# Performance work log

Hardware: AMD Instinct MI355X
Metric: run time of the kernel (lower is better)

Reference implementation:

```python
import jax, jax.numpy as jnp
import numpy as np

N = 100000      # nodes
E = 3200000     # edges (before self-loops)
F_IN = 512      # input features
HID = 16        # hidden dim (hard-coded in module)
C = 40          # classes
EPS = 1e-12     # F.normalize clamp


def setup_inputs() -> dict:
    key = jax.random.key(0)
    ks = jax.random.split(key, 5)
    x = jax.random.normal(ks[0], (N, F_IN), dtype=jnp.float32)
    edge_index = jax.random.randint(ks[1], (2, E), 0, N, dtype=jnp.int32)
    W1 = jax.random.normal(ks[2], (F_IN, HID), dtype=jnp.float32) / np.sqrt(F_IN)
    b1 = jnp.zeros((HID,), jnp.float32)
    W2 = jax.random.normal(ks[3], (HID, C), dtype=jnp.float32) / np.sqrt(HID)
    b2 = jnp.zeros((C,), jnp.float32)
    beta2 = jnp.ones((), jnp.float32)  # learnable beta of prop2 (init 1.0)
    return {"x": x, "edge_index": edge_index, "W1": W1, "b1": b1,
            "W2": W2, "b2": b2, "beta2": beta2}


def agnn_prop(x, src, dst, beta):
    # x: [N, d]; src/dst: [E'] with self-loops already appended
    norm = jnp.sqrt(jnp.sum(x * x, axis=-1, keepdims=True))
    xn = x / jnp.maximum(norm, EPS)                      # L2 normalize
    alpha = beta * jnp.sum(xn[src] * xn[dst], axis=-1)   # [E'] cosine sim * beta
    # segment softmax over edges grouped by destination node
    amax = jax.ops.segment_max(alpha, dst, num_segments=N)
    amax = jax.lax.stop_gradient(amax)
    ex = jnp.exp(alpha - amax[dst])
    denom = jax.ops.segment_sum(ex, dst, num_segments=N)
    w = ex / denom[dst]                                  # [E']
    return jax.ops.segment_sum(w[:, None] * x[src], dst, num_segments=N)


def reference(x, edge_index, W1, b1, W2, b2, beta2):
    # dropout is identity in eval mode
    h = jax.nn.relu(x @ W1 + b1)                         # [N, 16]
    loops = jnp.arange(N, dtype=edge_index.dtype)
    src = jnp.concatenate([edge_index[0], loops])        # add self-loops (PyG default)
    dst = jnp.concatenate([edge_index[1], loops])
    h = agnn_prop(h, src, dst, jnp.float32(1.0))         # prop1: fixed beta=1
    h = agnn_prop(h, src, dst, beta2)                    # prop2: learnable beta
    logits = h @ W2 + b2                                 # [N, 40]
    return jax.nn.log_softmax(logits, axis=-1)
```

## Files before the change

### kernel.cpp

```cpp
#include <hip/hip_runtime.h>
#include <hip/hip_bf16.h>

#define FIN 512
#define HID 16
#define NCLS 40
#define MAXNB 1024
#define NBLK 256

typedef unsigned short u16;
typedef __attribute__((ext_vector_type(8))) short short8;
typedef __attribute__((ext_vector_type(4))) float f32x4;

__device__ __forceinline__ float bf2f(u16 u) {
    return __uint_as_float(((unsigned int)u) << 16);
}
__device__ __forceinline__ u16 f2bf_rne(float f) {
    unsigned int u = __float_as_uint(f);
    unsigned int r = u + 0x7FFFu + ((u >> 16) & 1u);
    return (u16)(r >> 16);
}
__device__ __forceinline__ float load_in(const void* p, size_t i, int isf32) {
    return isf32 ? ((const float*)p)[i] : bf2f(((const u16*)p)[i]);
}

__global__ void probe_kernel(const unsigned int* __restrict__ x, int* __restrict__ flag)
{
    int cnt = 0;
    for (int i = threadIdx.x; i < 256; i += 64) {
        unsigned int w = x[i];
        float v = __uint_as_float((w & 0xFFFFu) << 16);
        float a = fabsf(v);
        if (a >= 6.1e-5f && a <= 64.f) cnt++;
    }
    #pragma unroll
    for (int off = 32; off >= 1; off >>= 1) cnt += __shfl_xor(cnt, off, 64);
    if (threadIdx.x == 0) *flag = (cnt < 128) ? 1 : 0;
}

__global__ __launch_bounds__(256) void gemm1_mfma(
    const void* __restrict__ x, const void* __restrict__ W1, const void* __restrict__ b1,
    float* __restrict__ h, float* __restrict__ rn, int ngroups, int N,
    const int* __restrict__ flagp)
{
    const int isf32 = *flagp;
    __shared__ u16 w1s[8192];
    __shared__ float b1s[HID];
    const int lane = threadIdx.x & 63;
    const int m    = lane & 15;
    const int quad = lane >> 4;

    for (int i = threadIdx.x; i < 8192; i += 256) {
        int kb = i >> 9, rem = i & 511, ln = rem >> 3, j = rem & 7;
        int k = kb*32 + (ln >> 4)*8 + j;
        w1s[i] = f2bf_rne(load_in(W1, (size_t)k*HID + (ln & 15), isf32));
    }
    if (threadIdx.x < HID) b1s[threadIdx.x] = load_in(b1, threadIdx.x, isf32);
    __syncthreads();

    const int wid = blockIdx.x * 4 + (threadIdx.x >> 6);
    const int nw  = gridDim.x * 4;
    const float bias = b1s[m];

    for (int g = wid; g < ngroups; g += nw) {
        size_t row = (size_t)g*16 + m;
        if (row >= (size_t)N) row = N - 1;
        f32x4 acc = {0.f, 0.f, 0.f, 0.f};
        if (isf32) {
            const float* xb = (const float*)x + row*FIN + quad*8;
            #pragma unroll
            for (int kb = 0; kb < 16; ++kb) {
                f32x4 v0 = *(const f32x4*)(xb + kb*32);
                f32x4 v1 = *(const f32x4*)(xb + kb*32 + 4);
                short8 a;
                a[0] = (short)f2bf_rne(v0[0]); a[1] = (short)f2bf_rne(v0[1]);
                a[2] = (short)f2bf_rne(v0[2]); a[3] = (short)f2bf_rne(v0[3]);
                a[4] = (short)f2bf_rne(v1[0]); a[5] = (short)f2bf_rne(v1[1]);
                a[6] = (short)f2bf_rne(v1[2]); a[7] = (short)f2bf_rne(v1[3]);
                short8 bf = *(const short8*)&w1s[kb*512 + lane*8];
                acc = __builtin_amdgcn_mfma_f32_16x16x32_bf16(a, bf, acc, 0, 0, 0);
            }
        } else {
            const u16* xb = (const u16*)x + row*FIN + quad*8;
            #pragma unroll
            for (int kb = 0; kb < 16; ++kb) {
                short8 a = *(const short8*)(xb + kb*32);
                short8 bf = *(const short8*)&w1s[kb*512 + lane*8];
                acc = __builtin_amdgcn_mfma_f32_16x16x32_bf16(a, bf, acc, 0, 0, 0);
            }
        }
        #pragma unroll
        for (int i = 0; i < 4; ++i) {
            int r = quad*4 + i;
            float v = fmaxf(acc[i] + bias, 0.f);
            size_t orow = (size_t)g*16 + r;
            if (orow < (size_t)N) h[orow*HID + m] = v;
            float ss = v*v;
            ss += __shfl_xor(ss, 1, 64);
            ss += __shfl_xor(ss, 2, 64);
            ss += __shfl_xor(ss, 4, 64);
            ss += __shfl_xor(ss, 8, 64);
            if (m == 0 && orow < (size_t)N) rn[orow] = 1.0f / fmaxf(sqrtf(ss), 1e-12f);
        }
    }
}

__global__ __launch_bounds__(256) void hist2d_kernel(
    const int* __restrict__ dst, int* __restrict__ blkhist, int E, int NB)
{
    __shared__ int hist[MAXNB];
    int t = threadIdx.x;
    for (int i = t; i < NB; i += 256) hist[i] = 0;
    __syncthreads();
    int chunk = (E + gridDim.x - 1) / gridDim.x;
    int beg = blockIdx.x * chunk;
    int end = min(E, beg + chunk);
    for (int i = beg + t; i < end; i += 256)
        atomicAdd(&hist[dst[i] >> 7], 1);
    __syncthreads();
    for (int i = t; i < NB; i += 256)
        blkhist[blockIdx.x * NB + i] = hist[i];
}

__global__ __launch_bounds__(256) void scanB_kernel(
    int* __restrict__ blkhist, int* __restrict__ bcnt, int NB)
{
    int b = blockIdx.x * 4 + (threadIdx.x >> 6);
    if (b >= NB) return;
    int lane = threadIdx.x & 63;
    int run = 0;
    for (int i0 = 0; i0 < NBLK; i0 += 64) {
        int idx = (i0 + lane) * NB + b;
        int v = blkhist[idx];
        int s = v;
        #pragma unroll
        for (int d = 1; d <= 32; d <<= 1) {
            int u = __shfl_up(s, d, 64);
            if (lane >= d) s += u;
        }
        blkhist[idx] = run + s - v;
        run += __shfl(s, 63, 64);
    }
    if (lane == 0) bcnt[b] = run;
}

__global__ __launch_bounds__(1024) void scan_kernel(
    const int* __restrict__ in, int* __restrict__ out, int n)
{
    __shared__ int buf[1024];
    __shared__ int carry;
    int t = threadIdx.x;
    if (t == 0) carry = 0;
    __syncthreads();
    for (int base = 0; base < n; base += 1024) {
        int v = (base + t < n) ? in[base + t] : 0;
        buf[t] = v;
        __syncthreads();
        for (int d = 1; d < 1024; d <<= 1) {
            int x = (t >= d) ? buf[t - d] : 0;
            __syncthreads();
            buf[t] += x;
            __syncthreads();
        }
        if (base + t < n) out[base + t] = carry + buf[t] - v;
        __syncthreads();
        if (t == 0) carry += buf[1023];
        __syncthreads();
    }
}

__global__ __launch_bounds__(256) void scatter_part_kernel(
    const int* __restrict__ src, const int* __restrict__ dst,
    const int* __restrict__ bbase, const int* __restrict__ blkhist,
    int* __restrict__ pairs, int E, int NB)
{
    __shared__ int base[MAXNB];
    __shared__ int cur[MAXNB];
    int t = threadIdx.x;
    for (int i = t; i < NB; i += 256) {
        base[i] = bbase[i] + blkhist[blockIdx.x * NB + i];
        cur[i] = 0;
    }
    __syncthreads();
    int chunk = (E + gridDim.x - 1) / gridDim.x;
    int beg = blockIdx.x * chunk;
    int end = min(E, beg + chunk);
    for (int i = beg + t; i < end; i += 256) {
        int d = dst[i], s = src[i];
        int b = d >> 7;
        int r = atomicAdd(&cur[b], 1);
        pairs[base[b] + r] = ((d & 127) << 24) | s;
    }
}

__global__ __launch_bounds__(256) void bucket_fill_kernel(
    const int* __restrict__ pairs, const int* __restrict__ bbase,
    const int* __restrict__ bcnt, int* __restrict__ row_start,
    int* __restrict__ counts, int* __restrict__ csr, int N)
{
    int b = blockIdx.x, n0 = b << 7;
    __shared__ int lhist[128], loff[128], lcur[128];
    int t = threadIdx.x;
    if (t < 128) { lhist[t] = 0; lcur[t] = 0; }
    __syncthreads();
    int base = bbase[b], cnt = bcnt[b];
    for (int i = t; i < cnt; i += 256)
        atomicAdd(&lhist[((unsigned)pairs[base + i]) >> 24], 1);
    __syncthreads();
    if (t < 64) {
        int c0 = lhist[2*t], c1 = lhist[2*t + 1];
        int tp = c0 + c1, s = tp;
        #pragma unroll
        for (int d = 1; d <= 32; d <<= 1) {
            int u = __shfl_up(s, d, 64);
            if (t >= d) s += u;
        }
        int excl = s - tp;
        loff[2*t] = excl; loff[2*t + 1] = excl + c0;
        int na = n0 + 2*t, nb2 = na + 1;
        if (na < N)  { row_start[na]  = base + excl;      counts[na]  = c0; }
        if (nb2 < N) { row_start[nb2] = base + excl + c0; counts[nb2] = c1; }
    }
    __syncthreads();
    for (int i = t; i < cnt; i += 256) {
        int w = pairs[base + i];
        int s = w & 0xFFFFFF, l = ((unsigned)w) >> 24;
        int p = atomicAdd(&lcur[l], 1);
        csr[base + loff[l] + p] = s;
    }
}

__global__ __launch_bounds__(256) void count_kernel(
    const int* __restrict__ dst, int* __restrict__ counts, int E)
{
    int e = blockIdx.x * 256 + threadIdx.x;
    if (e < E) atomicAdd(&counts[dst[e]], 1);
}

__global__ __launch_bounds__(256) void alloc_kernel(
    const int* __restrict__ counts, int* __restrict__ row_start,
    int* __restrict__ gcur, int N)
{
    int n = blockIdx.x * 256 + threadIdx.x;
    int lane = threadIdx.x & 63;
    int cnt = (n < N) ? counts[n] : 0;
    int s = cnt;
    #pragma unroll
    for (int d = 1; d <= 32; d <<= 1) {
        int t = __shfl_up(s, d, 64);
        if (lane >= d) s += t;
    }
    int total = __shfl(s, 63, 64);
    int base = 0;
    if (lane == 0) base = atomicAdd(gcur, total);
    base = __shfl(base, 0, 64);
    if (n < N) row_start[n] = base + s - cnt;
}

__global__ __launch_bounds__(256) void fill_kernel(
    const int* __restrict__ src, const int* __restrict__ dst,
    const int* __restrict__ row_start, int* __restrict__ cursor,
    int* __restrict__ csr, int E)
{
    int e = blockIdx.x * 256 + threadIdx.x;
    if (e < E) {
        int d = dst[e];
        int p = atomicAdd(&cursor[d], 1);
        csr[row_start[d] + p] = src[e];
    }
}

__global__ __launch_bounds__(256) void prop_kernel(
    const float* __restrict__ f, const float* __restrict__ rn,
    const int* __restrict__ row_start, const int* __restrict__ counts,
    const int* __restrict__ csr, const void* __restrict__ beta_ptr, int use_beta,
    float* __restrict__ out, float* __restrict__ rn_out, int N,
    const int* __restrict__ flagp)
{
    int wid = blockIdx.x * 4 + (threadIdx.x >> 6);
    if (wid >= N) return;
    const int isf32 = *flagp;
    const int lane = threadIdx.x & 63;
    const int sub  = lane & 3;
    const int es   = lane >> 2;
    const int n = wid;

    const float beta = use_beta ? load_in(beta_ptr, 0, isf32) : 1.0f;
    const float M = fabsf(beta);
    const f32x4 fn_v = *(const f32x4*)&f[(size_t)n*HID + sub*4];
    const float rn_n = rn[n];
    const int base = row_start[n];
    const int deg  = counts[n];

    f32x4 acc = {0.f, 0.f, 0.f, 0.f};
    float s = 0.f;
    for (int j0 = 0; j0 < deg + 1; j0 += 16) {
        int j = j0 + es;
        int idx = base + ((j < deg) ? j : 0);
        int v = csr[idx];
        int src = (j < deg) ? v : n;
        f32x4 fs = *(const f32x4*)&f[(size_t)src*HID + sub*4];
        float rs = rn[src];
        float p = fs[0]*fn_v[0] + fs[1]*fn_v[1] + fs[2]*fn_v[2] + fs[3]*fn_v[3];
        p += __shfl_xor(p, 1, 64);
        p += __shfl_xor(p, 2, 64);
        float alpha = beta * p * rs * rn_n;
        float t = (j <= deg) ? __expf(alpha - M) : 0.f;
        s += t;
        acc[0] += t*fs[0]; acc[1] += t*fs[1];
        acc[2] += t*fs[2]; acc[3] += t*fs[3];
    }
    #pragma unroll
    for (int off = 4; off <= 32; off <<= 1) {
        s      += __shfl_xor(s,      off, 64);
        acc[0] += __shfl_xor(acc[0], off, 64);
        acc[1] += __shfl_xor(acc[1], off, 64);
        acc[2] += __shfl_xor(acc[2], off, 64);
        acc[3] += __shfl_xor(acc[3], off, 64);
    }
    f32x4 o;
    o[0] = acc[0]/s; o[1] = acc[1]/s; o[2] = acc[2]/s; o[3] = acc[3]/s;
    if (lane < 4) *(f32x4*)&out[(size_t)n*HID + sub*4] = o;
    float p2 = o[0]*o[0] + o[1]*o[1] + o[2]*o[2] + o[3]*o[3];
    p2 += __shfl_xor(p2, 1, 64);
    p2 += __shfl_xor(p2, 2, 64);
    if (lane == 0) rn_out[n] = 1.0f / fmaxf(sqrtf(p2), 1e-12f);
}

__global__ __launch_bounds__(256) void classify_kernel(
    const float* __restrict__ h2, const void* __restrict__ W2,
    const void* __restrict__ b2, void* __restrict__ out, int N,
    const int* __restrict__ flagp)
{
    const int isf32 = *flagp;
    __shared__ float w2s[HID * NCLS];
    __shared__ float b2s[NCLS];
    for (int i = threadIdx.x; i < HID * NCLS; i += 256) w2s[i] = load_in(W2, i, isf32);
    if (threadIdx.x < NCLS) b2s[threadIdx.x] = load_in(b2, threadIdx.x, isf32);
    __syncthreads();

    int wid = blockIdx.x * 4 + (threadIdx.x >> 6);
    if (wid >= N) return;
    const int lane = threadIdx.x & 63;
    const int n = wid;

    float acc = -3.0e38f;
    if (lane < NCLS) {
        acc = b2s[lane];
        #pragma unroll
        for (int k = 0; k < HID; ++k)
            acc += h2[(size_t)n*HID + k] * w2s[k*NCLS + lane];
    }
    float mx = acc;
    #pragma unroll
    for (int off = 32; off >= 1; off >>= 1)
        mx = fmaxf(mx, __shfl_xor(mx, off, 64));
    float e = (lane < NCLS) ? __expf(acc - mx) : 0.f;
    float sum = e;
    #pragma unroll
    for (int off = 32; off >= 1; off >>= 1)
        sum += __shfl_xor(sum, off, 64);
    if (lane < NCLS) {
        float res = acc - mx - __logf(sum);
        if (!(res == res) || fabsf(res) > 1e30f) res = 0.f;
        size_t oi = (size_t)n*NCLS + lane;
        if (isf32) ((float*)out)[oi] = res;
        else       ((u16*)out)[oi]  = f2bf_rne(res);
    }
}

extern "C" void kernel_launch(void* const* d_in, const int* in_sizes, int n_in,
                              void* d_out, int out_size, void* d_ws, size_t ws_size,
                              hipStream_t stream)
{
    const void* x     = d_in[0];
    const int*  ei    = (const int*)d_in[1];
    const void* W1    = d_in[2];
    const void* b1    = d_in[3];
    const void* W2    = d_in[4];
    const void* b2    = d_in[5];
    const void* beta2 = d_in[6];

    const int N = in_sizes[0] / FIN;
    const int E = in_sizes[1] / 2;
    const int NB = (N + 127) >> 7;
    const int* srcv = ei;
    const int* dstv = ei + E;

    char* ws = (char*)d_ws;
    size_t off = 0;
    auto take = [&](size_t bytes) -> char* {
        char* p = ws + off;
        off += (bytes + 255) & ~(size_t)255;
        return p;
    };
    float* h0        = (float*)take((size_t)N * HID * 4);
    float* rn0       = (float*)take((size_t)N * 4);
    int*   counts    = (int*)take((size_t)N * 4);
    int*   cursor    = (int*)take((size_t)N * 4);
    int*   gcur      = (int*)take(256);
    int*   row_start = (int*)take((size_t)N * 4);
    int*   bcnt      = (int*)take((size_t)NB * 4);
    int*   bbase     = (int*)take((size_t)NB * 4);
    int*   csr       = (int*)take((size_t)(E + 64) * 4);
    int*   flag      = (int*)take(256);
    int*   pairs     = (int*)take((size_t)(E + 64) * 4);
    int*   blkhist   = (int*)take((size_t)NBLK * NB * 4);
    const int use_bucket = (off <= ws_size && NB <= MAXNB && N <= (1 << 24)) ? 1 : 0;

    float* h1  = (float*)d_out;
    float* rn1 = (float*)((char*)d_out + (size_t)N * HID * 4);
    float* h2  = h0;
    float* rn2 = rn0;

    size_t zbytes = (size_t)((char*)gcur - (char*)counts) + 256;
    hipMemsetAsync(counts, 0, zbytes, stream);

    probe_kernel<<<1, 64, 0, stream>>>((const unsigned int*)x, flag);

    const int ngroups = (N + 15) / 16;
    gemm1_mfma<<<(ngroups + 3) / 4, 256, 0, stream>>>(x, W1, b1, h0, rn0, ngroups, N, flag);

    int eb = (E + 255) / 256;
    int nb = (N + 255) / 256;
    int wb = (N + 3) / 4;
    if (use_bucket) {
        hist2d_kernel<<<NBLK, 256, 0, stream>>>(dstv, blkhist, E, NB);
        scanB_kernel<<<(NB + 3) / 4, 256, 0, stream>>>(blkhist, bcnt, NB);
        scan_kernel<<<1, 1024, 0, stream>>>(bcnt, bbase, NB);
        scatter_part_kernel<<<NBLK, 256, 0, stream>>>(srcv, dstv, bbase, blkhist, pairs, E, NB);
        bucket_fill_kernel<<<NB, 256, 0, stream>>>(pairs, bbase, bcnt, row_start, counts, csr, N);
    } else {
        count_kernel<<<eb, 256, 0, stream>>>(dstv, counts, E);
        alloc_kernel<<<nb, 256, 0, stream>>>(counts, row_start, gcur, N);
        fill_kernel<<<eb, 256, 0, stream>>>(srcv, dstv, row_start, cursor, csr, E);
    }

    prop_kernel<<<wb, 256, 0, stream>>>(h0, rn0, row_start, counts, csr,
                                        b1, 0, h1, rn1, N, flag);
    prop_kernel<<<wb, 256, 0, stream>>>(h1, rn1, row_start, counts, csr,
                                        beta2, 1, h2, rn2, N, flag);

    classify_kernel<<<wb, 256, 0, stream>>>(h2, W2, b2, d_out, N, flag);
}
```

Baseline: 583.6 us.

## Fuse second propagation with classifier and use packed bf16 conversion

Merges the second AGNN propagation with the linear classifier and log-softmax into one kernel. The propagated 16-dim row is broadcast across the wave with shuffles instead of being written to memory and read back, which removes one launch and the round trip of the h2 and rn2 buffers. h1 and rn1 now live in the workspace rather than the output buffer. Separately, the fp32-to-bf16 conversion in the first GEMM uses the packed v_cvt_pk_bf16_f32 instruction in place of manual rounding.

```diff
diff --git a/kernel.cpp b/kernel.cpp
--- a/kernel.cpp
+++ b/kernel.cpp
@@ -18,6 +18,11 @@
     unsigned int u = __float_as_uint(f);
     unsigned int r = u + 0x7FFFu + ((u >> 16) & 1u);
     return (u16)(r >> 16);
+}
+__device__ __forceinline__ unsigned int cvt_pk_bf16(float lo, float hi) {
+    unsigned int w;
+    asm("v_cvt_pk_bf16_f32 %0, %1, %2" : "=v"(w) : "v"(lo), "v"(hi));
+    return w;
 }
 __device__ __forceinline__ float load_in(const void* p, size_t i, int isf32) {
     return isf32 ? ((const float*)p)[i] : bf2f(((const u16*)p)[i]);
@@ -71,13 +76,13 @@
             for (int kb = 0; kb < 16; ++kb) {
                 f32x4 v0 = *(const f32x4*)(xb + kb*32);
                 f32x4 v1 = *(const f32x4*)(xb + kb*32 + 4);
-                short8 a;
-                a[0] = (short)f2bf_rne(v0[0]); a[1] = (short)f2bf_rne(v0[1]);
-                a[2] = (short)f2bf_rne(v0[2]); a[3] = (short)f2bf_rne(v0[3]);
-                a[4] = (short)f2bf_rne(v1[0]); a[5] = (short)f2bf_rne(v1[1]);
-                a[6] = (short)f2bf_rne(v1[2]); a[7] = (short)f2bf_rne(v1[3]);
+                union { unsigned int u[4]; short8 s; } cv;
+                cv.u[0] = cvt_pk_bf16(v0[0], v0[1]);
+                cv.u[1] = cvt_pk_bf16(v0[2], v0[3]);
+                cv.u[2] = cvt_pk_bf16(v1[0], v1[1]);
+                cv.u[3] = cvt_pk_bf16(v1[2], v1[3]);
                 short8 bf = *(const short8*)&w1s[kb*512 + lane*8];
-                acc = __builtin_amdgcn_mfma_f32_16x16x32_bf16(a, bf, acc, 0, 0, 0);
+                acc = __builtin_amdgcn_mfma_f32_16x16x32_bf16(cv.s, bf, acc, 0, 0, 0);
             }
         } else {
             const u16* xb = (const u16*)x + row*FIN + quad*8;
@@ -326,10 +331,12 @@
     if (lane == 0) rn_out[n] = 1.0f / fmaxf(sqrtf(p2), 1e-12f);
 }
 
-__global__ __launch_bounds__(256) void classify_kernel(
-    const float* __restrict__ h2, const void* __restrict__ W2,
-    const void* __restrict__ b2, void* __restrict__ out, int N,
-    const int* __restrict__ flagp)
+__global__ __launch_bounds__(256) void prop_cls_kernel(
+    const float* __restrict__ f, const float* __restrict__ rn,
+    const int* __restrict__ row_start, const int* __restrict__ counts,
+    const int* __restrict__ csr, const void* __restrict__ beta_ptr,
+    const void* __restrict__ W2, const void* __restrict__ b2,
+    void* __restrict__ outp, int N, const int* __restrict__ flagp)
 {
     const int isf32 = *flagp;
     __shared__ float w2s[HID * NCLS];
@@ -341,30 +348,77 @@
     int wid = blockIdx.x * 4 + (threadIdx.x >> 6);
     if (wid >= N) return;
     const int lane = threadIdx.x & 63;
+    const int sub  = lane & 3;
+    const int es   = lane >> 2;
     const int n = wid;
 
-    float acc = -3.0e38f;
+    const float beta = load_in(beta_ptr, 0, isf32);
+    const float M = fabsf(beta);
+    const f32x4 fn_v = *(const f32x4*)&f[(size_t)n*HID + sub*4];
+    const float rn_n = rn[n];
+    const int base = row_start[n];
+    const int deg  = counts[n];
+
+    f32x4 acc = {0.f, 0.f, 0.f, 0.f};
+    float s = 0.f;
+    for (int j0 = 0; j0 < deg + 1; j0 += 16) {
+        int j = j0 + es;
+        int idx = base + ((j < deg) ? j : 0);
+        int v = csr[idx];
+        int src = (j < deg) ? v : n;
+        f32x4 fs = *(const f32x4*)&f[(size_t)src*HID + sub*4];
+        float rs = rn[src];
+        float p = fs[0]*fn_v[0] + fs[1]*fn_v[1] + fs[2]*fn_v[2] + fs[3]*fn_v[3];
+        p += __shfl_xor(p, 1, 64);
+        p += __shfl_xor(p, 2, 64);
+        float alpha = beta * p * rs * rn_n;
+        float t = (j <= deg) ? __expf(alpha - M) : 0.f;
+        s += t;
+        acc[0] += t*fs[0]; acc[1] += t*fs[1];
+        acc[2] += t*fs[2]; acc[3] += t*fs[3];
+    }
+    #pragma unroll
+    for (int off = 4; off <= 32; off <<= 1) {
+        s      += __shfl_xor(s,      off, 64);
+        acc[0] += __shfl_xor(acc[0], off, 64);
+        acc[1] += __shfl_xor(acc[1], off, 64);
+        acc[2] += __shfl_xor(acc[2], off, 64);
+        acc[3] += __shfl_xor(acc[3], off, 64);
+    }
+    f32x4 o;
+    o[0] = acc[0]/s; o[1] = acc[1]/s; o[2] = acc[2]/s; o[3] = acc[3]/s;
+
+    float hall[16];
+    const int bl = lane & ~3;
+    #pragma unroll
+    for (int s2 = 0; s2 < 4; ++s2) {
+        hall[s2*4+0] = __shfl(o[0], bl + s2, 64);
+        hall[s2*4+1] = __shfl(o[1], bl + s2, 64);
+        hall[s2*4+2] = __shfl(o[2], bl + s2, 64);
+        hall[s2*4+3] = __shfl(o[3], bl + s2, 64);
+    }
+    float a2 = -3.0e38f;
     if (lane < NCLS) {
-        acc = b2s[lane];
+        a2 = b2s[lane];
         #pragma unroll
         for (int k = 0; k < HID; ++k)
-            acc += h2[(size_t)n*HID + k] * w2s[k*NCLS + lane];
-    }
-    float mx = acc;
+            a2 += hall[k] * w2s[k*NCLS + lane];
+    }
+    float mx = a2;
     #pragma unroll
     for (int off = 32; off >= 1; off >>= 1)
         mx = fmaxf(mx, __shfl_xor(mx, off, 64));
-    float e = (lane < NCLS) ? __expf(acc - mx) : 0.f;
+    float e = (lane < NCLS) ? __expf(a2 - mx) : 0.f;
     float sum = e;
     #pragma unroll
     for (int off = 32; off >= 1; off >>= 1)
         sum += __shfl_xor(sum, off, 64);
     if (lane < NCLS) {
-        float res = acc - mx - __logf(sum);
+        float res = a2 - mx - __logf(sum);
         if (!(res == res) || fabsf(res) > 1e30f) res = 0.f;
         size_t oi = (size_t)n*NCLS + lane;
-        if (isf32) ((float*)out)[oi] = res;
-        else       ((u16*)out)[oi]  = f2bf_rne(res);
+        if (isf32) ((float*)outp)[oi] = res;
+        else       ((u16*)outp)[oi]  = f2bf_rne(res);
     }
 }
 
@@ -395,6 +449,8 @@
     };
     float* h0        = (float*)take((size_t)N * HID * 4);
     float* rn0       = (float*)take((size_t)N * 4);
+    float* h1        = (float*)take((size_t)N * HID * 4);
+    float* rn1       = (float*)take((size_t)N * 4);
     int*   counts    = (int*)take((size_t)N * 4);
     int*   cursor    = (int*)take((size_t)N * 4);
     int*   gcur      = (int*)take(256);
@@ -406,11 +462,6 @@
     int*   pairs     = (int*)take((size_t)(E + 64) * 4);
     int*   blkhist   = (int*)take((size_t)NBLK * NB * 4);
     const int use_bucket = (off <= ws_size && NB <= MAXNB && N <= (1 << 24)) ? 1 : 0;
-
-    float* h1  = (float*)d_out;
-    float* rn1 = (float*)((char*)d_out + (size_t)N * HID * 4);
-    float* h2  = h0;
-    float* rn2 = rn0;
 
     size_t zbytes = (size_t)((char*)gcur - (char*)counts) + 256;
     hipMemsetAsync(counts, 0, zbytes, stream);
@@ -437,8 +488,6 @@
 
     prop_kernel<<<wb, 256, 0, stream>>>(h0, rn0, row_start, counts, csr,
                                         b1, 0, h1, rn1, N, flag);
-    prop_kernel<<<wb, 256, 0, stream>>>(h1, rn1, row_start, counts, csr,
-                                        beta2, 1, h2, rn2, N, flag);
-
-    classify_kernel<<<wb, 256, 0, stream>>>(h2, W2, b2, d_out, N, flag);
-}
+    prop_cls_kernel<<<wb, 256, 0, stream>>>(h1, rn1, row_start, counts, csr,
+                                            beta2, W2, b2, d_out, N, flag);
+}
```

New measurement: 575.2 us. About the same (-1.5%).
